# Optimization experiments

Hardware: AMD Instinct MI355X
Metric: run time of the kernel (lower is better)

## Reference

```python
import jax, jax.numpy as jnp
import numpy as np

N_RAYS = 16384
MAX_STEPS = 512          # fixed march-step budget per ray (dense-padded packed samples)
GRID_R = 128             # occupancy grid resolution
NEAR = 0.05
FAR = 3.0
STEP = (FAR - NEAR) / MAX_STEPS   # render_step_size


def setup_inputs() -> dict:
    key = jax.random.key(0)
    k1, k2, k3 = jax.random.split(key, 3)
    rays_o = jax.random.uniform(k1, (N_RAYS, 3), minval=-0.5, maxval=0.5, dtype=jnp.float32)
    d = jax.random.normal(k2, (N_RAYS, 3), dtype=jnp.float32)
    rays_d = d / jnp.linalg.norm(d, axis=-1, keepdims=True)
    aabb = jnp.array([[-1.0, -1.0, -1.0], [1.0, 1.0, 1.0]], dtype=jnp.float32)
    occ_grid = jax.random.bernoulli(k3, 0.3, (GRID_R, GRID_R, GRID_R))  # bool occupancy
    return {"rays_o": rays_o, "rays_d": rays_d, "aabb": aabb, "occ_grid": occ_grid}


def reference(rays_o, rays_d, aabb, occ_grid):
    # --- ray / AABB intersection (per-ray valid t interval) ---
    safe_d = jnp.where(jnp.abs(rays_d) > 1e-10, rays_d, 1e-10)
    inv_d = 1.0 / safe_d
    t0 = (aabb[0] - rays_o) * inv_d          # [N,3]
    t1 = (aabb[1] - rays_o) * inv_d
    tmin = jnp.maximum(jnp.max(jnp.minimum(t0, t1), axis=-1), NEAR)   # [N]
    tmax = jnp.minimum(jnp.min(jnp.maximum(t0, t1), axis=-1), FAR)    # [N]

    # --- uniform marching bins (cone_angle = 0) ---
    edges = NEAR + jnp.arange(MAX_STEPS + 1, dtype=rays_o.dtype) * STEP
    starts = edges[:-1]                      # [S]
    ends = edges[1:]                         # [S]
    mids = 0.5 * (starts + ends)             # [S]

    # sample midpoint positions: [N,S,3]
    pos = rays_o[:, None, :] + rays_d[:, None, :] * mids[None, :, None]

    # --- occupancy-grid lookup (irregular gather) ---
    scale = (pos - aabb[0]) / (aabb[1] - aabb[0])          # [N,S,3] in [0,1) if inside
    idx = jnp.clip((scale * GRID_R).astype(jnp.int32), 0, GRID_R - 1)
    occ = occ_grid[idx[..., 0], idx[..., 1], idx[..., 2]]  # [N,S] bool
    inside = jnp.all((scale >= 0.0) & (scale < 1.0), axis=-1)

    valid = (starts[None, :] >= tmin[:, None]) & (ends[None, :] <= tmax[:, None]) & occ & inside  # [N,S]

    # --- packed_info (exclusive cumsum of per-ray counts) ---
    counts = valid.sum(axis=1).astype(jnp.int32)            # [N]
    offsets = jnp.concatenate([jnp.zeros((1,), jnp.int32), jnp.cumsum(counts)[:-1].astype(jnp.int32)])
    packed_info = jnp.stack([offsets, counts], axis=1)      # [N,2]

    # --- unpack_info equivalent: per-sample ray index, then irregular gather ---
    ray_indices = jnp.broadcast_to(jnp.arange(N_RAYS, dtype=jnp.int32)[:, None],
                                   (N_RAYS, MAX_STEPS)).reshape(-1)  # [N*S]
    mask = valid.reshape(-1)                                 # [N*S]
    maskf = mask.astype(rays_o.dtype)[:, None]

    origins = rays_o[ray_indices] * maskf                    # [N*S,3]
    dirs = rays_d[ray_indices] * maskf                       # [N*S,3]
    s_flat = jnp.where(mask, jnp.broadcast_to(starts, (N_RAYS, MAX_STEPS)).reshape(-1), 0.0)
    e_flat = jnp.where(mask, jnp.broadcast_to(ends, (N_RAYS, MAX_STEPS)).reshape(-1), 0.0)

    return origins, dirs, s_flat, e_flat, packed_info, ray_indices, mask
```

## Files before the change

kernel.cpp:

```cpp
#include <hip/hip_runtime.h>

#define N_RAYS 16384
#define MAX_STEPS 512
#define GRID_R 128
#define NS (N_RAYS * MAX_STEPS)

__global__ void detect_dtype(const void* __restrict__ occ, int* __restrict__ flag) {
    __shared__ int ok_int, ok_flt;
    if (threadIdx.x == 0) { ok_int = 1; ok_flt = 1; }
    __syncthreads();
    const int*   pi = (const int*)occ;
    const float* pf = (const float*)occ;
    for (int i = threadIdx.x; i < 1024; i += blockDim.x) {
        int v = pi[i];
        if (v != 0 && v != 1) atomicAnd(&ok_int, 0);
        float f = pf[i];
        if (!(f == 0.0f || f == 1.0f)) atomicAnd(&ok_flt, 0);
    }
    __syncthreads();
    if (threadIdx.x == 0) flag[0] = ok_int ? 0 : (ok_flt ? 1 : 2);
}

__global__ __launch_bounds__(512)
void sample_kernel(const float* __restrict__ rays_o, const float* __restrict__ rays_d,
                   const float* __restrict__ aabb, const void* __restrict__ occ,
                   const int* __restrict__ flag_p, float* __restrict__ out,
                   int* __restrict__ counts)
{
    const int r = blockIdx.x;
    const int s = threadIdx.x;
    const int mode = flag_p[0];

    const float ox = rays_o[3 * r + 0], oy = rays_o[3 * r + 1], oz = rays_o[3 * r + 2];
    const float dx = rays_d[3 * r + 0], dy = rays_d[3 * r + 1], dz = rays_d[3 * r + 2];
    const float a0x = aabb[0], a0y = aabb[1], a0z = aabb[2];
    const float a1x = aabb[3], a1y = aabb[4], a1z = aabb[5];

    const float sdx = (fabsf(dx) > 1e-10f) ? dx : 1e-10f;
    const float sdy = (fabsf(dy) > 1e-10f) ? dy : 1e-10f;
    const float sdz = (fabsf(dz) > 1e-10f) ? dz : 1e-10f;
    const float invx = __fdiv_rn(1.0f, sdx);
    const float invy = __fdiv_rn(1.0f, sdy);
    const float invz = __fdiv_rn(1.0f, sdz);

    const float t0x = __fmul_rn(__fsub_rn(a0x, ox), invx);
    const float t1x = __fmul_rn(__fsub_rn(a1x, ox), invx);
    const float t0y = __fmul_rn(__fsub_rn(a0y, oy), invy);
    const float t1y = __fmul_rn(__fsub_rn(a1y, oy), invy);
    const float t0z = __fmul_rn(__fsub_rn(a0z, oz), invz);
    const float t1z = __fmul_rn(__fsub_rn(a1z, oz), invz);

    const float tmin = fmaxf(fmaxf(fmaxf(fminf(t0x, t1x), fminf(t0y, t1y)), fminf(t0z, t1z)), 0.05f);
    const float tmax = fminf(fminf(fminf(fmaxf(t0x, t1x), fmaxf(t0y, t1y)), fmaxf(t0z, t1z)), 3.0f);

    const float step_f = (float)((3.0 - 0.05) / 512.0);
    const float start = __fadd_rn(0.05f, __fmul_rn((float)s, step_f));
    const float end   = __fadd_rn(0.05f, __fmul_rn((float)(s + 1), step_f));
    const float mid   = __fmul_rn(0.5f, __fadd_rn(start, end));

    const float px = __fadd_rn(ox, __fmul_rn(dx, mid));
    const float py = __fadd_rn(oy, __fmul_rn(dy, mid));
    const float pz = __fadd_rn(oz, __fmul_rn(dz, mid));

    const float scx = __fdiv_rn(__fsub_rn(px, a0x), __fsub_rn(a1x, a0x));
    const float scy = __fdiv_rn(__fsub_rn(py, a0y), __fsub_rn(a1y, a0y));
    const float scz = __fdiv_rn(__fsub_rn(pz, a0z), __fsub_rn(a1z, a0z));

    const bool inside = (scx >= 0.0f) && (scx < 1.0f) &&
                        (scy >= 0.0f) && (scy < 1.0f) &&
                        (scz >= 0.0f) && (scz < 1.0f);
    const bool geom = inside && (start >= tmin) && (end <= tmax);

    bool valid = false;
    if (geom) {
        int gx = (int)__fmul_rn(scx, (float)GRID_R);
        int gy = (int)__fmul_rn(scy, (float)GRID_R);
        int gz = (int)__fmul_rn(scz, (float)GRID_R);
        gx = min(max(gx, 0), GRID_R - 1);
        gy = min(max(gy, 0), GRID_R - 1);
        gz = min(max(gz, 0), GRID_R - 1);
        const int lin = (gx * GRID_R + gy) * GRID_R + gz;
        bool occv;
        if (mode == 0)      occv = ((const int*)occ)[lin] != 0;
        else if (mode == 1) occv = ((const float*)occ)[lin] != 0.0f;
        else                occv = ((const unsigned char*)occ)[lin] != 0;
        valid = occv;
    }

    const int i = (r << 9) | s;
    float* og = out;
    float* dr = out + 3L * NS;
    float* sf = out + 6L * NS;
    float* ef = out + 7L * NS;
    float* ri = out + 8L * NS + 2L * N_RAYS;
    float* mk = ri + (long)NS;

    og[3 * i + 0] = valid ? ox : 0.0f;
    og[3 * i + 1] = valid ? oy : 0.0f;
    og[3 * i + 2] = valid ? oz : 0.0f;
    dr[3 * i + 0] = valid ? dx : 0.0f;
    dr[3 * i + 1] = valid ? dy : 0.0f;
    dr[3 * i + 2] = valid ? dz : 0.0f;
    sf[i] = valid ? start : 0.0f;
    ef[i] = valid ? end : 0.0f;
    ri[i] = (float)r;
    mk[i] = valid ? 1.0f : 0.0f;

    const unsigned long long b = __ballot(valid);
    __shared__ int wcount[8];
    if ((threadIdx.x & 63) == 0) wcount[threadIdx.x >> 6] = __popcll(b);
    __syncthreads();
    if (threadIdx.x == 0) {
        int t = 0;
#pragma unroll
        for (int w = 0; w < 8; ++w) t += wcount[w];
        counts[r] = t;
    }
}

__global__ __launch_bounds__(1024)
void scan_kernel(const int* __restrict__ counts, float* __restrict__ packed)
{
    __shared__ int partial[1024];
    const int tid = threadIdx.x;
    const int base = tid * 16;
    int sum = 0;
#pragma unroll
    for (int i = 0; i < 16; ++i) sum += counts[base + i];
    partial[tid] = sum;
    __syncthreads();
    for (int off = 1; off < 1024; off <<= 1) {
        int v = (tid >= off) ? partial[tid - off] : 0;
        __syncthreads();
        partial[tid] += v;
        __syncthreads();
    }
    int run = (tid == 0) ? 0 : partial[tid - 1];
#pragma unroll
    for (int i = 0; i < 16; ++i) {
        const int c = counts[base + i];
        packed[2 * (base + i) + 0] = (float)run;
        packed[2 * (base + i) + 1] = (float)c;
        run += c;
    }
}

extern "C" void kernel_launch(void* const* d_in, const int* in_sizes, int n_in,
                              void* d_out, int out_size, void* d_ws, size_t ws_size,
                              hipStream_t stream) {
    const float* rays_o = (const float*)d_in[0];
    const float* rays_d = (const float*)d_in[1];
    const float* aabb   = (const float*)d_in[2];
    const void*  occ    = d_in[3];
    float* out = (float*)d_out;

    int* flag   = (int*)d_ws;
    int* counts = (int*)d_ws + 16;

    detect_dtype<<<1, 256, 0, stream>>>(occ, flag);
    sample_kernel<<<N_RAYS, 512, 0, stream>>>(rays_o, rays_d, aabb, occ, flag, out, counts);
    scan_kernel<<<1, 1024, 0, stream>>>(counts, out + 8L * NS);
}
```

Before: 356.5 us.

## Pack occupancy grid into bitmask and vectorize output stores via shared mask

Adds a pre-pass that packs the occupancy grid into a 256 KB bitmask in workspace, so the per-sample gather reads bits that fit in cache instead of a full-size grid. The per-sample output writes are also restructured: the validity mask goes to shared memory and threads write origins, directions, starts, ends, ray indices and mask as coalesced float4 stores instead of stride-3 scalar stores. The price is an extra kernel launch, a workspace-size dependency that falls back to the old gather path, and more index arithmetic in the store phase.

```diff
diff --git a/kernel.cpp b/kernel.cpp
--- a/kernel.cpp
+++ b/kernel.cpp
@@ -3,7 +3,12 @@
 #define N_RAYS 16384
 #define MAX_STEPS 512
 #define GRID_R 128
+#define N_CELLS (GRID_R * GRID_R * GRID_R)
 #define NS (N_RAYS * MAX_STEPS)
+
+#define WS_COUNTS_OFF 1024
+#define WS_BITS_OFF 131072
+#define WS_NEEDED (WS_BITS_OFF + N_CELLS / 8)
 
 __global__ void detect_dtype(const void* __restrict__ occ, int* __restrict__ flag) {
     __shared__ int ok_int, ok_flt;
@@ -21,15 +26,28 @@
     if (threadIdx.x == 0) flag[0] = ok_int ? 0 : (ok_flt ? 1 : 2);
 }
 
+__global__ __launch_bounds__(256)
+void pack_occ(const void* __restrict__ occ, const int* __restrict__ flag_p,
+              unsigned long long* __restrict__ bits) {
+    const int mode = flag_p[0];
+    const int idx = blockIdx.x * 256 + threadIdx.x;
+    bool v;
+    if (mode == 0)      v = ((const int*)occ)[idx] != 0;
+    else if (mode == 1) v = ((const float*)occ)[idx] != 0.0f;
+    else                v = ((const unsigned char*)occ)[idx] != 0;
+    const unsigned long long b = __ballot(v);
+    if ((threadIdx.x & 63) == 0) bits[idx >> 6] = b;
+}
+
 __global__ __launch_bounds__(512)
 void sample_kernel(const float* __restrict__ rays_o, const float* __restrict__ rays_d,
                    const float* __restrict__ aabb, const void* __restrict__ occ,
-                   const int* __restrict__ flag_p, float* __restrict__ out,
-                   int* __restrict__ counts)
+                   const int* __restrict__ flag_p,
+                   const unsigned int* __restrict__ bits, int use_bits,
+                   float* __restrict__ out, int* __restrict__ counts)
 {
     const int r = blockIdx.x;
     const int s = threadIdx.x;
-    const int mode = flag_p[0];
 
     const float ox = rays_o[3 * r + 0], oy = rays_o[3 * r + 1], oz = rays_o[3 * r + 2];
     const float dx = rays_d[3 * r + 0], dy = rays_d[3 * r + 1], dz = rays_d[3 * r + 2];
@@ -80,37 +98,65 @@
         gy = min(max(gy, 0), GRID_R - 1);
         gz = min(max(gz, 0), GRID_R - 1);
         const int lin = (gx * GRID_R + gy) * GRID_R + gz;
-        bool occv;
-        if (mode == 0)      occv = ((const int*)occ)[lin] != 0;
-        else if (mode == 1) occv = ((const float*)occ)[lin] != 0.0f;
-        else                occv = ((const unsigned char*)occ)[lin] != 0;
-        valid = occv;
-    }
-
-    const int i = (r << 9) | s;
-    float* og = out;
-    float* dr = out + 3L * NS;
-    float* sf = out + 6L * NS;
-    float* ef = out + 7L * NS;
-    float* ri = out + 8L * NS + 2L * N_RAYS;
-    float* mk = ri + (long)NS;
-
-    og[3 * i + 0] = valid ? ox : 0.0f;
-    og[3 * i + 1] = valid ? oy : 0.0f;
-    og[3 * i + 2] = valid ? oz : 0.0f;
-    dr[3 * i + 0] = valid ? dx : 0.0f;
-    dr[3 * i + 1] = valid ? dy : 0.0f;
-    dr[3 * i + 2] = valid ? dz : 0.0f;
-    sf[i] = valid ? start : 0.0f;
-    ef[i] = valid ? end : 0.0f;
-    ri[i] = (float)r;
-    mk[i] = valid ? 1.0f : 0.0f;
-
+        if (use_bits) {
+            valid = (bits[lin >> 5] >> (lin & 31)) & 1u;
+        } else {
+            const int mode = flag_p[0];
+            if (mode == 0)      valid = ((const int*)occ)[lin] != 0;
+            else if (mode == 1) valid = ((const float*)occ)[lin] != 0.0f;
+            else                valid = ((const unsigned char*)occ)[lin] != 0;
+        }
+    }
+
+    __shared__ float lmask[512];
+    __shared__ int wcount[8];
+    lmask[s] = valid ? 1.0f : 0.0f;
     const unsigned long long b = __ballot(valid);
-    __shared__ int wcount[8];
-    if ((threadIdx.x & 63) == 0) wcount[threadIdx.x >> 6] = __popcll(b);
-    __syncthreads();
-    if (threadIdx.x == 0) {
+    if ((s & 63) == 0) wcount[s >> 6] = __popcll(b);
+    __syncthreads();
+
+    if (s < 384) {
+        const int f = 4 * s;
+        float4 vo, vd;
+#pragma unroll
+        for (int k = 0; k < 4; ++k) {
+            const int ff = f + k;
+            const int smp = ff / 3;
+            const int c = ff - smp * 3;
+            const float m = lmask[smp];
+            const float oc = (c == 0) ? ox : ((c == 1) ? oy : oz);
+            const float dc = (c == 0) ? dx : ((c == 1) ? dy : dz);
+            ((float*)&vo)[k] = __fmul_rn(m, oc);
+            ((float*)&vd)[k] = __fmul_rn(m, dc);
+        }
+        ((float4*)out)[(long)r * 384 + s] = vo;
+        ((float4*)(out + 3L * NS))[(long)r * 384 + s] = vd;
+    }
+
+    {
+        const int grp = s >> 7;
+        const int t = s & 127;
+        float4 v;
+#pragma unroll
+        for (int k = 0; k < 4; ++k) {
+            const int smp = 4 * t + k;
+            const float m = lmask[smp];
+            float val;
+            if (grp == 0)      val = __fmul_rn(m, __fadd_rn(0.05f, __fmul_rn((float)smp, step_f)));
+            else if (grp == 1) val = __fmul_rn(m, __fadd_rn(0.05f, __fmul_rn((float)(smp + 1), step_f)));
+            else if (grp == 2) val = (float)r;
+            else               val = m;
+            ((float*)&v)[k] = val;
+        }
+        float* basep;
+        if (grp == 0)      basep = out + 6L * NS;
+        else if (grp == 1) basep = out + 7L * NS;
+        else if (grp == 2) basep = out + 8L * NS + 2L * N_RAYS;
+        else               basep = out + 8L * NS + 2L * N_RAYS + (long)NS;
+        ((float4*)basep)[(long)r * 128 + t] = v;
+    }
+
+    if (s == 0) {
         int t = 0;
 #pragma unroll
         for (int w = 0; w < 8; ++w) t += wcount[w];
@@ -155,9 +201,15 @@
     float* out = (float*)d_out;
 
     int* flag   = (int*)d_ws;
-    int* counts = (int*)d_ws + 16;
+    int* counts = (int*)((char*)d_ws + WS_COUNTS_OFF);
+    unsigned long long* bits64 = (unsigned long long*)((char*)d_ws + WS_BITS_OFF);
+    const int use_bits = (ws_size >= (size_t)WS_NEEDED) ? 1 : 0;
 
     detect_dtype<<<1, 256, 0, stream>>>(occ, flag);
-    sample_kernel<<<N_RAYS, 512, 0, stream>>>(rays_o, rays_d, aabb, occ, flag, out, counts);
+    if (use_bits)
+        pack_occ<<<N_CELLS / 256, 256, 0, stream>>>(occ, flag, bits64);
+    sample_kernel<<<N_RAYS, 512, 0, stream>>>(rays_o, rays_d, aabb, occ, flag,
+                                              (const unsigned int*)bits64, use_bits,
+                                              out, counts);
     scan_kernel<<<1, 1024, 0, stream>>>(counts, out + 8L * NS);
 }
```

Result: no change. 353.9 us (-0.7%).
